# Optimization experiments

Hardware: AMD Instinct MI355X
Metric: run time of the kernel (lower is better)

Reference implementation:

```python
import jax, jax.numpy as jnp
import numpy as np
import math

INF = 100000.0
EPS = 1e-08


def setup_inputs() -> dict:
    key = jax.random.key(0)
    ks = jax.random.split(key, 12)
    B, N, c_n, c_z, C, H, Pq, Pv = 1, 768, 384, 128, 16, 12, 4, 8
    s = jax.random.normal(ks[0], (B, N, c_n), jnp.float32)
    z = jax.random.normal(ks[1], (B, N, N, c_z), jnp.float32)
    # proper rotation-ish frames via QR of random matrices
    m = jax.random.normal(ks[2], (B, N, 3, 3), jnp.float32)
    rot, _ = jnp.linalg.qr(m)
    trans = jax.random.normal(ks[3], (B, N, 3), jnp.float32) * 10.0
    pair_mask = jnp.ones((B, N, N), jnp.float32)

    def lin(k, fin, fout, scale=0.02):
        kw, kb = jax.random.split(k)
        w = jax.random.normal(kw, (fin, fout), jnp.float32) * scale
        b = jax.random.normal(kb, (fout,), jnp.float32) * scale
        return w, b

    wq, bq = lin(ks[4], c_n, H * C)
    wkv, bkv = lin(ks[5], c_n, 2 * H * C)
    wqp, bqp = lin(ks[6], c_n, H * Pq * 3)
    wkvp, bkvp = lin(ks[7], c_n, H * (Pq + Pv) * 3)
    wb, bb = lin(ks[8], c_z, H)
    head_weights = jnp.full((H,), 0.5413248546129181, jnp.float32)  # softplus^-1(1)
    concat_dim = H * (c_z + C + Pv * 4)
    wout, bout = lin(ks[9], concat_dim, c_n)
    return dict(s=s, z=z, rot=rot, trans=trans, pair_mask=pair_mask,
                wq=wq, bq=bq, wkv=wkv, bkv=bkv, wqp=wqp, bqp=bqp,
                wkvp=wkvp, bkvp=bkvp, wb=wb, bb=bb,
                head_weights=head_weights, wout=wout, bout=bout)


def reference(s, z, rot, trans, pair_mask, wq, bq, wkv, bkv, wqp, bqp,
              wkvp, bkvp, wb, bb, head_weights, wout, bout):
    B, N, _ = s.shape
    H = head_weights.shape[0]
    C = wq.shape[1] // H
    Pq = wqp.shape[1] // (3 * H)
    Ptot = wkvp.shape[1] // (3 * H)
    Pv = Ptot - Pq

    q = (s @ wq + bq).reshape(B, N, H, C)
    kv = (s @ wkv + bkv).reshape(B, N, H, 2 * C)
    k, v = kv[..., :C], kv[..., C:]

    def make_pts(x_flat, n):
        # torch: split last dim into 3 contiguous chunks (x..,y..,z..), stack -> [B,N,n,3]
        p = x_flat.reshape(B, N, 3, n).swapaxes(-1, -2)
        return jnp.einsum('bnij,bnpj->bnpi', rot, p) + trans[:, :, None, :]

    q_pts = make_pts(s @ wqp + bqp, H * Pq).reshape(B, N, H, Pq, 3)
    kv_pts = make_pts(s @ wkvp + bkvp, H * Ptot).reshape(B, N, H, Ptot, 3)
    k_pts, v_pts = kv_pts[..., :Pq, :], kv_pts[..., Pq:, :]

    b_bias = z @ wb + bb  # [B,N,N,H]
    a = jnp.einsum('bihc,bjhc->bhij', q, k) * math.sqrt(1.0 / (3 * C))
    a = a + math.sqrt(1.0 / 3.0) * b_bias.transpose(0, 3, 1, 2)

    # point attention: squared distances in global frame  [B,Ni,Nj,H,Pq]
    d2 = jnp.sum((q_pts[:, :, None] - k_pts[:, None]) ** 2, axis=-1)
    hw = jax.nn.softplus(head_weights) * math.sqrt(1.0 / (3.0 * (Pq * 9.0 / 2.0)))
    pt_att = -0.5 * jnp.sum(d2 * hw[:, None], axis=-1)  # [B,Ni,Nj,H]
    a = a + pt_att.transpose(0, 3, 1, 2)
    a = a + (INF * (pair_mask - 1.0))[:, None]
    a = jax.nn.softmax(a, axis=-1)  # [B,H,Ni,Nj]

    o = jnp.einsum('bhij,bjhc->bihc', a, v).reshape(B, N, H * C)

    o_pt = jnp.einsum('bhij,bjhpc->bihpc', a, v_pts)  # [B,N,H,Pv,3]
    # inverse rigid: R^T (x - t)
    o_pt = jnp.einsum('bnij,bnhpi->bnhpj', rot, o_pt - trans[:, :, None, None, :])
    o_pt_norm = jnp.sqrt(jnp.sum(o_pt ** 2, axis=-1) + EPS).reshape(B, N, H * Pv)
    o_pt = o_pt.reshape(B, N, H * Pv, 3)

    o_pair = jnp.einsum('bhij,bijc->bihc', a, z).reshape(B, N, -1)

    cat = jnp.concatenate(
        [o, o_pt[..., 0], o_pt[..., 1], o_pt[..., 2], o_pt_norm, o_pair], axis=-1)
    return cat @ wout + bout
```

## Files before the change

kernel.cpp:

```cpp
#include <hip/hip_runtime.h>
#include <hip/hip_bf16.h>

#define NRES 768
#define NN2  589824
#define CN   384
#define CZ   128
#define CH   16
#define NH   12
#define CATD 2112
#define LSTR 776

template<typename T> __device__ __forceinline__ float cvt(T x);
template<> __device__ __forceinline__ float cvt<float>(float x) { return x; }
template<> __device__ __forceinline__ float cvt<__hip_bfloat16>(__hip_bfloat16 x) { return __bfloat162float(x); }

template<typename T> struct Ld8;
template<> struct Ld8<float> {
    static __device__ __forceinline__ void go(const float* p, float* f) {
        const float4* q = (const float4*)p;
        float4 a = q[0], b = q[1];
        f[0]=a.x; f[1]=a.y; f[2]=a.z; f[3]=a.w;
        f[4]=b.x; f[5]=b.y; f[6]=b.z; f[7]=b.w;
    }
};
template<> struct Ld8<__hip_bfloat16> {
    static __device__ __forceinline__ void go(const __hip_bfloat16* p, float* f) {
        uint4 u = *(const uint4*)p;
        f[0]=__uint_as_float(u.x<<16); f[1]=__uint_as_float(u.x&0xffff0000u);
        f[2]=__uint_as_float(u.y<<16); f[3]=__uint_as_float(u.y&0xffff0000u);
        f[4]=__uint_as_float(u.z<<16); f[5]=__uint_as_float(u.z&0xffff0000u);
        f[6]=__uint_as_float(u.w<<16); f[7]=__uint_as_float(u.w&0xffff0000u);
    }
};

template<typename T> struct Ld4;
template<> struct Ld4<float> {
    static __device__ __forceinline__ void go(const float* p, float* f) {
        float4 a = *(const float4*)p;
        f[0]=a.x; f[1]=a.y; f[2]=a.z; f[3]=a.w;
    }
};
template<> struct Ld4<__hip_bfloat16> {
    static __device__ __forceinline__ void go(const __hip_bfloat16* p, float* f) {
        uint2 u = *(const uint2*)p;
        f[0]=__uint_as_float(u.x<<16); f[1]=__uint_as_float(u.x&0xffff0000u);
        f[2]=__uint_as_float(u.y<<16); f[3]=__uint_as_float(u.y&0xffff0000u);
    }
};

__device__ __forceinline__ bool detect_bf16(const void* pm) {
    const unsigned short* u = (const unsigned short*)pm;
    return (u[0] == 0x3F80u) && (u[1] == 0x3F80u);
}

template<typename T>
__device__ void proj_body(
    const T* __restrict__ s, const T* __restrict__ rot, const T* __restrict__ trans,
    const T* __restrict__ wq, const T* __restrict__ bq,
    const T* __restrict__ wkv, const T* __restrict__ bkv,
    const T* __restrict__ wqp, const T* __restrict__ bqp,
    const T* __restrict__ wkvp, const T* __restrict__ bkvp,
    float* __restrict__ qw, float* __restrict__ kt, float* __restrict__ vw,
    float* __restrict__ qpw, float* __restrict__ kpt, float* __restrict__ vpw,
    float* sL, float* rawL)
{
    const int n0 = blockIdx.x * 4;
    const int tid = threadIdx.x;

    for (int idx = tid; idx < 4 * CN; idx += 256)
        sL[idx] = cvt<T>(s[(size_t)n0 * CN + idx]);
    __syncthreads();

    for (int cq = tid; cq < 288; cq += 256) {
        const int col0 = cq * 4;
        const T* W; int stride, wcol0; const T* Bv;
        if (col0 < 192)      { W = wq;   stride = 192; wcol0 = col0;       Bv = bq;   }
        else if (col0 < 576) { W = wkv;  stride = 384; wcol0 = col0 - 192; Bv = bkv;  }
        else if (col0 < 720) { W = wqp;  stride = 144; wcol0 = col0 - 576; Bv = bqp;  }
        else                 { W = wkvp; stride = 432; wcol0 = col0 - 720; Bv = bkvp; }
        float b4[4];
        Ld4<T>::go(Bv + wcol0, b4);
        float a[4][4];
        #pragma unroll
        for (int r = 0; r < 4; ++r)
            #pragma unroll
            for (int e = 0; e < 4; ++e) a[r][e] = b4[e];
        #pragma unroll 4
        for (int kk = 0; kk < CN; ++kk) {
            float w4[4];
            Ld4<T>::go(W + (size_t)kk * stride + wcol0, w4);
            #pragma unroll
            for (int r = 0; r < 4; ++r) {
                const float sv = sL[r * CN + kk];
                a[r][0] += sv * w4[0];
                a[r][1] += sv * w4[1];
                a[r][2] += sv * w4[2];
                a[r][3] += sv * w4[3];
            }
        }
        #pragma unroll
        for (int e = 0; e < 4; ++e) {
            const int col = col0 + e;
            const int wcol = wcol0 + e;
            #pragma unroll
            for (int r = 0; r < 4; ++r) {
                const int n = n0 + r;
                const float val = a[r][e];
                if (col < 192) {
                    qw[(size_t)n * 192 + col] = val;
                } else if (col < 576) {
                    int hh = wcol >> 5, x = wcol & 31;
                    if (x < 16) kt[(size_t)(hh * 16 + x) * NRES + n] = val;
                    else        vw[(size_t)n * 192 + hh * 16 + (x - 16)] = val;
                } else if (col < 720) {
                    rawL[r * 576 + wcol] = val;
                } else {
                    rawL[r * 576 + 144 + wcol] = val;
                }
            }
        }
    }
    __syncthreads();

    for (int idx = tid; idx < 4 * 192; idx += 256) {
        const int r = idx / 192, p = idx % 192;
        const int n = n0 + r;
        float R[9], Tt[3];
        #pragma unroll
        for (int d = 0; d < 9; ++d) R[d] = cvt<T>(rot[(size_t)n * 9 + d]);
        #pragma unroll
        for (int d = 0; d < 3; ++d) Tt[d] = cvt<T>(trans[(size_t)n * 3 + d]);
        float lx, ly, lz;
        if (p < 48) {
            lx = rawL[r * 576 + p];
            ly = rawL[r * 576 + 48 + p];
            lz = rawL[r * 576 + 96 + p];
        } else {
            const int pk = p - 48;
            lx = rawL[r * 576 + 144 + pk];
            ly = rawL[r * 576 + 144 + 144 + pk];
            lz = rawL[r * 576 + 144 + 288 + pk];
        }
        const float gx = R[0] * lx + R[1] * ly + R[2] * lz + Tt[0];
        const float gy = R[3] * lx + R[4] * ly + R[5] * lz + Tt[1];
        const float gz = R[6] * lx + R[7] * ly + R[8] * lz + Tt[2];
        if (p < 48) {
            float* d = qpw + (size_t)n * 144 + p * 3;
            d[0] = gx; d[1] = gy; d[2] = gz;
        } else {
            const int pk = p - 48;
            const int hh = pk / 12, pp = pk % 12;
            if (pp < 4) {
                const int comp = (hh * 4 + pp) * 3;
                kpt[(size_t)(comp + 0) * NRES + n] = gx;
                kpt[(size_t)(comp + 1) * NRES + n] = gy;
                kpt[(size_t)(comp + 2) * NRES + n] = gz;
            } else {
                float* d = vpw + (size_t)n * 288 + (hh * 8 + (pp - 4)) * 3;
                d[0] = gx; d[1] = gy; d[2] = gz;
            }
        }
    }
}

__global__ __launch_bounds__(256) void k_proj(
    const void* s, const void* rot, const void* trans,
    const void* wq, const void* bq, const void* wkv, const void* bkv,
    const void* wqp, const void* bqp, const void* wkvp, const void* bkvp,
    const void* pm,
    float* qw, float* kt, float* vw, float* qpw, float* kpt, float* vpw)
{
    __shared__ float sL[4 * CN];
    __shared__ float rawL[4 * 576];
    if (detect_bf16(pm))
        proj_body<__hip_bfloat16>((const __hip_bfloat16*)s, (const __hip_bfloat16*)rot,
            (const __hip_bfloat16*)trans, (const __hip_bfloat16*)wq, (const __hip_bfloat16*)bq,
            (const __hip_bfloat16*)wkv, (const __hip_bfloat16*)bkv, (const __hip_bfloat16*)wqp,
            (const __hip_bfloat16*)bqp, (const __hip_bfloat16*)wkvp, (const __hip_bfloat16*)bkvp,
            qw, kt, vw, qpw, kpt, vpw, sL, rawL);
    else
        proj_body<float>((const float*)s, (const float*)rot, (const float*)trans,
            (const float*)wq, (const float*)bq, (const float*)wkv, (const float*)bkv,
            (const float*)wqp, (const float*)bqp, (const float*)wkvp, (const float*)bkvp,
            qw, kt, vw, qpw, kpt, vpw, sL, rawL);
}

template<typename T>
__device__ void bias_body(const T* __restrict__ z, const T* __restrict__ wb,
                          const T* __restrict__ bb, float* __restrict__ biasg,
                          float* zL, float* wbT, float* bbL, float* outL)
{
    const int tid = threadIdx.x;
    const size_t p0 = (size_t)blockIdx.x * 64;

    for (int idx = tid; idx < CZ * NH; idx += 256) {
        const int c = idx / NH, h = idx - c * NH;
        wbT[h * 132 + c] = cvt<T>(wb[idx]);
    }
    if (tid < NH) bbL[tid] = cvt<T>(bb[tid]);

    for (int v8 = tid; v8 < 64 * CZ / 8; v8 += 256) {
        float f[8];
        Ld8<T>::go(z + p0 * CZ + (size_t)v8 * 8, f);
        const int pp = v8 >> 4, cc = (v8 & 15) * 8;
        #pragma unroll
        for (int u = 0; u < 8; ++u) zL[pp * 132 + cc + u] = f[u];
    }
    __syncthreads();

    const float SB = 0.5773502691896258f;
    for (int o = tid; o < 64 * NH; o += 256) {
        const int pp = o / NH, h = o - pp * NH;
        const float* zr = &zL[pp * 132];
        const float* wr = &wbT[h * 132];
        float acc = bbL[h];
        #pragma unroll 8
        for (int c = 0; c < CZ; ++c) acc += zr[c] * wr[c];
        outL[h * 64 + pp] = SB * acc;
    }
    __syncthreads();

    for (int v4 = tid; v4 < 192; v4 += 256) {
        const int h = v4 / 16, pp4 = (v4 - h * 16) * 4;
        *(float4*)(biasg + (size_t)h * NN2 + p0 + pp4) = *(const float4*)&outL[h * 64 + pp4];
    }
}

__global__ __launch_bounds__(256) void k_bias(
    const void* z, const void* wb, const void* bb, const void* pm, float* biasg)
{
    __shared__ float zL[64 * 132];
    __shared__ float wbT[NH * 132];
    __shared__ float bbL[NH];
    __shared__ float outL[NH * 64];
    if (detect_bf16(pm))
        bias_body<__hip_bfloat16>((const __hip_bfloat16*)z, (const __hip_bfloat16*)wb,
                                  (const __hip_bfloat16*)bb, biasg, zL, wbT, bbL, outL);
    else
        bias_body<float>((const float*)z, (const float*)wb, (const float*)bb,
                         biasg, zL, wbT, bbL, outL);
}

template<typename T>
__device__ void attn_split_body(
    const T* __restrict__ pm, const T* __restrict__ hw,
    const float* __restrict__ qw, const float* __restrict__ kt,
    const float* __restrict__ qpw, const float* __restrict__ kpt,
    float* bA,
    float* L, float* qL, float* qpL, float* coefL)
{
    const int i = blockIdx.x, tid = threadIdx.x;

    if (tid < 192) qL[tid] = qw[(size_t)i * 192 + tid];
    if (tid < 144) qpL[tid] = qpw[(size_t)i * 144 + tid];
    if (tid < NH) {
        const float x = cvt<T>(hw[tid]);
        coefL[tid] = -0.5f * log1pf(__expf(x)) * 0.13608276348795434f;
    }
    __syncthreads();

    const float SQK = 0.14433756729740643f;

    for (int t = tid; t < 768; t += 256) {
        const int q = t % 192, g = t / 192;
        const int j0 = 4 * q;
        float mk[4];
        Ld4<T>::go(pm + (size_t)i * NRES + j0, mk);
        #pragma unroll
        for (int e = 0; e < 4; ++e) mk[e] = 100000.0f * (mk[e] - 1.0f);
        #pragma unroll
        for (int hh = 0; hh < 3; ++hh) {
            const int h = 3 * g + hh;
            const float4 b4 = *(const float4*)(bA + (size_t)h * NN2 + (size_t)i * NRES + j0);
            float4 qk = make_float4(0.f, 0.f, 0.f, 0.f);
            #pragma unroll
            for (int c = 0; c < CH; ++c) {
                const float qc = qL[h * CH + c];
                const float4 kv = *(const float4*)(kt + (size_t)(h * CH + c) * NRES + j0);
                qk.x += qc * kv.x; qk.y += qc * kv.y; qk.z += qc * kv.z; qk.w += qc * kv.w;
            }
            float4 dd = make_float4(0.f, 0.f, 0.f, 0.f);
            #pragma unroll
            for (int pc = 0; pc < 12; ++pc) {
                const float qp = qpL[h * 12 + pc];
                const float4 kp = *(const float4*)(kpt + (size_t)(h * 12 + pc) * NRES + j0);
                const float dx = qp - kp.x, dy = qp - kp.y, dz = qp - kp.z, dw = qp - kp.w;
                dd.x += dx * dx; dd.y += dy * dy; dd.z += dz * dz; dd.w += dw * dw;
            }
            const float cf = coefL[h];
            float4 o;
            o.x = SQK * qk.x + b4.x + cf * dd.x + mk[0];
            o.y = SQK * qk.y + b4.y + cf * dd.y + mk[1];
            o.z = SQK * qk.z + b4.z + cf * dd.z + mk[2];
            o.w = SQK * qk.w + b4.w + cf * dd.w + mk[3];
            *(float4*)&L[h * LSTR + j0] = o;
        }
    }
    __syncthreads();

    const int wave = tid >> 6, lane = tid & 63;
    for (int hh = 0; hh < 3; ++hh) {
        const int h = wave * 3 + hh;
        float m = -1e30f;
        for (int j = lane; j < NRES; j += 64) m = fmaxf(m, L[h * LSTR + j]);
        #pragma unroll
        for (int off = 32; off > 0; off >>= 1) m = fmaxf(m, __shfl_xor(m, off));
        float ssum = 0.f;
        for (int j = lane; j < NRES; j += 64) {
            const float e = __expf(L[h * LSTR + j] - m);
            L[h * LSTR + j] = e;
            ssum += e;
        }
        #pragma unroll
        for (int off = 32; off > 0; off >>= 1) ssum += __shfl_xor(ssum, off);
        const float inv = 1.0f / ssum;
        for (int j = lane; j < NRES; j += 64) L[h * LSTR + j] *= inv;
    }
    __syncthreads();

    for (int v = tid; v < 2304; v += 256) {
        const int h = v / 192, q = v - h * 192;
        *(float4*)(bA + (size_t)h * NN2 + (size_t)i * NRES + 4 * q)
            = *(const float4*)&L[h * LSTR + 4 * q];
    }
}

__global__ __launch_bounds__(256, 4) void k_attn_split(
    const void* pm, const void* hw,
    const float* qw, const float* kt, const float* qpw, const float* kpt,
    float* bA)
{
    __shared__ float L[NH * LSTR];
    __shared__ float qL[192];
    __shared__ float qpL[144];
    __shared__ float coefL[NH];
    if (detect_bf16(pm))
        attn_split_body<__hip_bfloat16>((const __hip_bfloat16*)pm,
            (const __hip_bfloat16*)hw, qw, kt, qpw, kpt, bA, L, qL, qpL, coefL);
    else
        attn_split_body<float>((const float*)pm,
            (const float*)hw, qw, kt, qpw, kpt, bA, L, qL, qpL, coefL);
}

template<typename T>
__device__ void av_body(const T* __restrict__ z, const T* __restrict__ rot,
                        const T* __restrict__ trans,
                        const float* __restrict__ Ag,
                        const float* __restrict__ vw, const float* __restrict__ vpw,
                        float* __restrict__ cat, float* buf, float* og)
{
    const int i = blockIdx.x, tid = threadIdx.x;

    for (int v = tid; v < 2304; v += 256) {
        const int h = v / 192, q = v - h * 192;
        const float4 rd = *(const float4*)(Ag + (size_t)h * NN2 + (size_t)i * NRES + 4 * q);
        buf[(4 * q + 0) * NH + h] = rd.x;
        buf[(4 * q + 1) * NH + h] = rd.y;
        buf[(4 * q + 2) * NH + h] = rd.z;
        buf[(4 * q + 3) * NH + h] = rd.w;
    }
    __syncthreads();

    const int lane5 = tid & 31;
    const int jg = tid >> 5;
    const int j0 = jg * 96;

    float4 pacc[NH];
    #pragma unroll
    for (int h = 0; h < NH; ++h) pacc[h] = make_float4(0.f, 0.f, 0.f, 0.f);

    float4 vacc[4];
    const float* vbase[4]; int vstr[4], hsel[4]; bool vok[4];
    #pragma unroll
    for (int k = 0; k < 4; ++k) {
        int m = lane5 + 32 * k;
        vok[k] = (m < 120);
        if (!vok[k]) m = 0;
        const int h = m / 10, q = m - h * 10;
        hsel[k] = h;
        if (q < 4) { vbase[k] = vw  + h * 16 + 4 * q;       vstr[k] = 192; }
        else       { vbase[k] = vpw + h * 24 + 4 * (q - 4); vstr[k] = 288; }
        vacc[k] = make_float4(0.f, 0.f, 0.f, 0.f);
    }

    const T* zr = z + (size_t)i * NRES * CZ;
    for (int j = j0; j < j0 + 96; ++j) {
        float f[4];
        Ld4<T>::go(zr + (size_t)j * CZ + lane5 * 4, f);
        const float4* ar = (const float4*)&buf[j * NH];
        const float4 a0 = ar[0], a1 = ar[1], a2 = ar[2];
        const float av[NH] = {a0.x,a0.y,a0.z,a0.w, a1.x,a1.y,a1.z,a1.w, a2.x,a2.y,a2.z,a2.w};
        #pragma unroll
        for (int h = 0; h < NH; ++h) {
            pacc[h].x += av[h] * f[0];
            pacc[h].y += av[h] * f[1];
            pacc[h].z += av[h] * f[2];
            pacc[h].w += av[h] * f[3];
        }
        #pragma unroll
        for (int k = 0; k < 4; ++k) {
            const float4 vv = *(const float4*)(vbase[k] + (size_t)j * vstr[k]);
            const float a = buf[j * NH + hsel[k]];
            vacc[k].x += a * vv.x;
            vacc[k].y += a * vv.y;
            vacc[k].z += a * vv.z;
            vacc[k].w += a * vv.w;
        }
    }
    __syncthreads();

    #pragma unroll
    for (int h = 0; h < NH; ++h)
        *(float4*)&buf[(jg * NH + h) * CZ + lane5 * 4] = pacc[h];
    __syncthreads();
    float* crow = cat + (size_t)i * CATD + 576;
    for (int o = tid; o < NH * CZ; o += 256) {
        float s = 0.f;
        #pragma unroll
        for (int g = 0; g < 8; ++g) s += buf[g * NH * CZ + o];
        crow[o] = s;
    }
    __syncthreads();

    #pragma unroll
    for (int k = 0; k < 4; ++k)
        if (vok[k]) *(float4*)&buf[jg * 480 + (lane5 + 32 * k) * 4] = vacc[k];
    __syncthreads();
    for (int o = tid; o < 480; o += 256) {
        float s = 0.f;
        #pragma unroll
        for (int g = 0; g < 8; ++g) s += buf[g * 480 + o];
        const int h = o / 40, t = o - h * 40;
        if (t < 16) cat[(size_t)i * CATD + h * 16 + t] = s;
        else        og[h * 24 + (t - 16)] = s;
    }
    __syncthreads();

    if (tid < 96) {
        const int h = tid >> 3, p = tid & 7;
        float R[9], Tt[3];
        #pragma unroll
        for (int d = 0; d < 9; ++d) R[d] = cvt<T>(rot[(size_t)i * 9 + d]);
        #pragma unroll
        for (int d = 0; d < 3; ++d) Tt[d] = cvt<T>(trans[(size_t)i * 3 + d]);
        const float gx = og[h * 24 + p * 3 + 0] - Tt[0];
        const float gy = og[h * 24 + p * 3 + 1] - Tt[1];
        const float gz = og[h * 24 + p * 3 + 2] - Tt[2];
        const float lx = R[0] * gx + R[3] * gy + R[6] * gz;
        const float ly = R[1] * gx + R[4] * gy + R[7] * gz;
        const float lz = R[2] * gx + R[5] * gy + R[8] * gz;
        const float nrm = sqrtf(lx * lx + ly * ly + lz * lz + 1e-8f);
        float* cr = cat + (size_t)i * CATD;
        cr[192 + tid] = lx;
        cr[288 + tid] = ly;
        cr[384 + tid] = lz;
        cr[480 + tid] = nrm;
    }
}

__global__ __launch_bounds__(256) void k_av(
    const void* z, const void* pm, const void* rot, const void* trans,
    const float* Ag, const float* vw, const float* vpw, float* cat)
{
    __shared__ float buf[8 * NH * CZ];
    __shared__ float og[288];
    if (detect_bf16(pm))
        av_body<__hip_bfloat16>((const __hip_bfloat16*)z, (const __hip_bfloat16*)rot,
                                (const __hip_bfloat16*)trans, Ag, vw, vpw, cat, buf, og);
    else
        av_body<float>((const float*)z, (const float*)rot, (const float*)trans,
                       Ag, vw, vpw, cat, buf, og);
}

template<typename T>
__device__ void attn_fused_body(
    const T* __restrict__ z, const T* __restrict__ pm,
    const T* __restrict__ wb, const T* __restrict__ bb, const T* __restrict__ hw,
    const T* __restrict__ rot, const T* __restrict__ trans,
    const float* __restrict__ qw, const float* __restrict__ kt,
    const float* __restrict__ qpw, const float* __restrict__ kpt,
    const float* __restrict__ vw, const float* __restrict__ vpw,
    float* __restrict__ cat,
    float* L, float* wbL, float* qL, float* qpL, float* coefL, float* bbL,
    float* og, float* opairL)
{
    const int i = blockIdx.x, tid = threadIdx.x;

    for (int idx = tid; idx < CZ * NH; idx += 256) wbL[idx] = cvt<T>(wb[idx]);
    if (tid < 192) qL[tid] = qw[(size_t)i * 192 + tid];
    if (tid < 144) qpL[tid] = qpw[(size_t)i * 144 + tid];
    if (tid < NH) {
        const float x = cvt<T>(hw[tid]);
        coefL[tid] = -0.5f * log1pf(__expf(x)) * 0.13608276348795434f;
        bbL[tid] = cvt<T>(bb[tid]);
    }
    __syncthreads();

    const float SQK = 0.14433756729740643f;
    const float SB  = 0.5773502691896258f;

    for (int j = tid; j < NRES; j += 256) {
        const T* zr = z + ((size_t)i * NRES + j) * CZ;
        float bias[NH];
        #pragma unroll
        for (int h = 0; h < NH; ++h) bias[h] = 0.f;
        for (int cb = 0; cb < 16; ++cb) {
            float zf[8];
            Ld8<T>::go(zr + cb * 8, zf);
            #pragma unroll
            for (int uu = 0; uu < 8; ++uu) {
                const float* wrow = &wbL[(cb * 8 + uu) * NH];
                const float zc = zf[uu];
                #pragma unroll
                for (int h = 0; h < NH; ++h) bias[h] += zc * wrow[h];
            }
        }
        const float maskoff = 100000.0f * (cvt<T>(pm[(size_t)i * NRES + j]) - 1.0f);
        #pragma unroll
        for (int h = 0; h < NH; ++h) {
            float qk = 0.f;
            #pragma unroll
            for (int c = 0; c < CH; ++c)
                qk += qL[h * CH + c] * kt[(size_t)(h * CH + c) * NRES + j];
            float d2s = 0.f;
            #pragma unroll
            for (int pc = 0; pc < 12; ++pc) {
                const float diff = qpL[h * 12 + pc] - kpt[(size_t)(h * 12 + pc) * NRES + j];
                d2s += diff * diff;
            }
            L[h * NRES + j] = SQK * qk + SB * (bias[h] + bbL[h]) + coefL[h] * d2s + maskoff;
        }
    }
    __syncthreads();

    const int wave = tid >> 6, lane = tid & 63;
    for (int hh = 0; hh < 3; ++hh) {
        const int h = wave * 3 + hh;
        float m = -1e30f;
        for (int j = lane; j < NRES; j += 64) m = fmaxf(m, L[h * NRES + j]);
        #pragma unroll
        for (int off = 32; off > 0; off >>= 1) m = fmaxf(m, __shfl_xor(m, off));
        float ssum = 0.f;
        for (int j = lane; j < NRES; j += 64) {
            const float e = __expf(L[h * NRES + j] - m);
            L[h * NRES + j] = e;
            ssum += e;
        }
        #pragma unroll
        for (int off = 32; off > 0; off >>= 1) ssum += __shfl_xor(ssum, off);
        const float inv = 1.0f / ssum;
        for (int j = lane; j < NRES; j += 64) L[h * NRES + j] *= inv;
    }
    __syncthreads();

    for (int oc = tid; oc < 480; oc += 256) {
        float acc = 0.f;
        if (oc < 192) {
            const int h = oc >> 4;
            const float* Lh = &L[h * NRES];
            #pragma unroll 4
            for (int j = 0; j < NRES; ++j) acc += Lh[j] * vw[(size_t)j * 192 + oc];
            cat[(size_t)i * CATD + oc] = acc;
        } else {
            const int t = oc - 192;
            const int h = t / 24;
            const float* Lh = &L[h * NRES];
            #pragma unroll 4
            for (int j = 0; j < NRES; ++j) acc += Lh[j] * vpw[(size_t)j * 288 + t];
            og[t] = acc;
        }
    }
    __syncthreads();

    if (tid < 96) {
        const int h = tid >> 3, p = tid & 7;
        float R[9], Tt[3];
        #pragma unroll
        for (int d = 0; d < 9; ++d) R[d] = cvt<T>(rot[(size_t)i * 9 + d]);
        #pragma unroll
        for (int d = 0; d < 3; ++d) Tt[d] = cvt<T>(trans[(size_t)i * 3 + d]);
        const float gx = og[h * 24 + p * 3 + 0] - Tt[0];
        const float gy = og[h * 24 + p * 3 + 1] - Tt[1];
        const float gz = og[h * 24 + p * 3 + 2] - Tt[2];
        const float lx = R[0] * gx + R[3] * gy + R[6] * gz;
        const float ly = R[1] * gx + R[4] * gy + R[7] * gz;
        const float lz = R[2] * gx + R[5] * gy + R[8] * gz;
        const float nrm = sqrtf(lx * lx + ly * ly + lz * lz + 1e-8f);
        float* cr = cat + (size_t)i * CATD;
        cr[192 + tid] = lx;
        cr[288 + tid] = ly;
        cr[384 + tid] = lz;
        cr[480 + tid] = nrm;
    }

    const int c = tid & 127, half = tid >> 7;
    float acc[NH];
    #pragma unroll
    for (int h = 0; h < NH; ++h) acc[h] = 0.f;
    const T* zi = z + (size_t)i * NRES * CZ;
    for (int j = half * 384; j < half * 384 + 384; ++j) {
        const float zv = cvt<T>(zi[(size_t)j * CZ + c]);
        #pragma unroll
        for (int h = 0; h < NH; ++h) acc[h] += L[h * NRES + j] * zv;
    }
    if (half == 0) {
        #pragma unroll
        for (int h = 0; h < NH; ++h) opairL[h * CZ + c] = acc[h];
    }
    __syncthreads();
    if (half == 1) {
        #pragma unroll
        for (int h = 0; h < NH; ++h) opairL[h * CZ + c] += acc[h];
    }
    __syncthreads();
    float* crow = cat + (size_t)i * CATD + 576;
    for (int idx = tid; idx < NH * CZ; idx += 256) crow[idx] = opairL[idx];
}

__global__ __launch_bounds__(256) void k_attn_fused(
    const void* z, const void* pm, const void* wb, const void* bb, const void* hw,
    const void* rot, const void* trans,
    const float* qw, const float* kt, const float* qpw, const float* kpt,
    const float* vw, const float* vpw, float* cat)
{
    __shared__ float L[NH * NRES];
    __shared__ float wbL[CZ * NH];
    __shared__ float qL[192];
    __shared__ float qpL[144];
    __shared__ float coefL[NH], bbL[NH];
    __shared__ float og[288];
    __shared__ float opairL[NH * CZ];
    if (detect_bf16(pm))
        attn_fused_body<__hip_bfloat16>((const __hip_bfloat16*)z, (const __hip_bfloat16*)pm,
            (const __hip_bfloat16*)wb, (const __hip_bfloat16*)bb, (const __hip_bfloat16*)hw,
            (const __hip_bfloat16*)rot, (const __hip_bfloat16*)trans,
            qw, kt, qpw, kpt, vw, vpw, cat, L, wbL, qL, qpL, coefL, bbL, og, opairL);
    else
        attn_fused_body<float>((const float*)z, (const float*)pm,
            (const float*)wb, (const float*)bb, (const float*)hw,
            (const float*)rot, (const float*)trans,
            qw, kt, qpw, kpt, vw, vpw, cat, L, wbL, qL, qpL, coefL, bbL, og, opairL);
}

template<typename T>
__device__ void out_body(const float* __restrict__ cat, const T* __restrict__ wout,
                         const T* __restrict__ bout, T* __restrict__ out,
                         float* catL, float* red)
{
    const int i0 = blockIdx.x * 4, tid = threadIdx.x;
    {
        const float4* src = (const float4*)(cat + (size_t)i0 * CATD);
        float4* dst = (float4*)catL;
        for (int v = tid; v < CATD; v += 384) dst[v] = src[v];
    }
    __syncthreads();

    const int cq = tid % 96, kg = tid / 96;
    const int c0 = cq * 4;
    const int k0 = kg * 528;
    float a[4][4];
    #pragma unroll
    for (int r = 0; r < 4; ++r)
        #pragma unroll
        for (int e = 0; e < 4; ++e) a[r][e] = 0.f;

    #pragma unroll 4
    for (int kk = k0; kk < k0 + 528; ++kk) {
        float w4[4];
        Ld4<T>::go(wout + (size_t)kk * CN + c0, w4);
        #pragma unroll
        for (int r = 0; r < 4; ++r) {
            const float cv = catL[r * CATD + kk];
            a[r][0] += cv * w4[0];
            a[r][1] += cv * w4[1];
            a[r][2] += cv * w4[2];
            a[r][3] += cv * w4[3];
        }
    }
    #pragma unroll
    for (int r = 0; r < 4; ++r)
        *(float4*)&red[(kg * 4 + r) * CN + c0] = make_float4(a[r][0], a[r][1], a[r][2], a[r][3]);
    __syncthreads();

    for (int o = tid; o < 4 * CN; o += 384) {
        const int r = o / CN, col = o - r * CN;
        float s = red[(0 * 4 + r) * CN + col] + red[(1 * 4 + r) * CN + col]
                + red[(2 * 4 + r) * CN + col] + red[(3 * 4 + r) * CN + col];
        out[(size_t)(i0 + r) * CN + col] = (T)(s + cvt<T>(bout[col]));
    }
}

__global__ __launch_bounds__(384) void k_out(
    const float* cat, const void* wout, const void* bout, void* out, const void* pm)
{
    __shared__ float catL[4 * CATD];
    __shared__ float red[16 * CN];
    if (detect_bf16(pm))
        out_body<__hip_bfloat16>(cat, (const __hip_bfloat16*)wout,
                                 (const __hip_bfloat16*)bout, (__hip_bfloat16*)out, catL, red);
    else
        out_body<float>(cat, (const float*)wout, (const float*)bout, (float*)out, catL, red);
}

extern "C" void kernel_launch(void* const* d_in, const int* in_sizes, int n_in,
                              void* d_out, int out_size, void* d_ws, size_t ws_size,
                              hipStream_t stream) {
    const void* s         = d_in[0];
    const void* z         = d_in[1];
    const void* rot       = d_in[2];
    const void* trans     = d_in[3];
    const void* pair_mask = d_in[4];
    const void* wq        = d_in[5];
    const void* bq        = d_in[6];
    const void* wkv       = d_in[7];
    const void* bkv       = d_in[8];
    const void* wqp       = d_in[9];
    const void* bqp       = d_in[10];
    const void* wkvp      = d_in[11];
    const void* bkvp      = d_in[12];
    const void* wb        = d_in[13];
    const void* bb        = d_in[14];
    const void* hw        = d_in[15];
    const void* wout      = d_in[16];
    const void* bout      = d_in[17];

    float* ws  = (float*)d_ws;
    float* qw  = ws;
    float* kt  = qw  + (size_t)NRES * 192;
    float* vw  = kt  + (size_t)NRES * 192;
    float* qpw = vw  + (size_t)NRES * 192;
    float* kpt = qpw + (size_t)NRES * 144;
    float* vpw = kpt + (size_t)NRES * 144;
    float* cat = vpw + (size_t)NRES * 288;
    float* bA  = cat + (size_t)NRES * CATD;

    const size_t need_split = ((size_t)2506752 + 7077888) * sizeof(float);

    k_proj<<<NRES / 4, 256, 0, stream>>>(s, rot, trans, wq, bq, wkv, bkv,
                                         wqp, bqp, wkvp, bkvp, pair_mask,
                                         qw, kt, vw, qpw, kpt, vpw);
    if (ws_size >= need_split) {
        k_bias<<<(NRES * NRES) / 64, 256, 0, stream>>>(z, wb, bb, pair_mask, bA);
        k_attn_split<<<NRES, 256, 0, stream>>>(pair_mask, hw,
                                               qw, kt, qpw, kpt, bA);
        k_av<<<NRES, 256, 0, stream>>>(z, pair_mask, rot, trans,
                                       bA, vw, vpw, cat);
    } else {
        k_attn_fused<<<NRES, 256, 0, stream>>>(z, pair_mask, wb, bb, hw, rot, trans,
                                               qw, kt, qpw, kpt, vw, vpw, cat);
    }
    k_out<<<NRES / 4, 384, 0, stream>>>(cat, wout, bout, d_out, pair_mask);
}
```

Before: 850.1 us.

## Retile projection, bias and output kernels for more parallelism and register reuse

The projection kernel now gives each block a single residue instead of four, launching 768 blocks for more parallelism at the cost of reloading the weights four times as often. The pair-bias kernel drops its shared-memory staging of z: each thread keeps a quarter of a row in registers and the partial dot products are combined with warp shuffles. The output GEMM moves to 8 columns per thread with float4 reads from shared memory, splits K eight ways and reduces in two stages. Several shared arrays gain 16-byte alignment so the vector accesses are valid.

```diff
diff --git a/kernel.cpp b/kernel.cpp
--- a/kernel.cpp
+++ b/kernel.cpp
@@ -64,11 +64,11 @@
     float* __restrict__ qpw, float* __restrict__ kpt, float* __restrict__ vpw,
     float* sL, float* rawL)
 {
-    const int n0 = blockIdx.x * 4;
+    const int n = blockIdx.x;
     const int tid = threadIdx.x;
 
-    for (int idx = tid; idx < 4 * CN; idx += 256)
-        sL[idx] = cvt<T>(s[(size_t)n0 * CN + idx]);
+    for (int idx = tid; idx < CN; idx += 256)
+        sL[idx] = cvt<T>(s[(size_t)n * CN + idx]);
     __syncthreads();
 
     for (int cq = tid; cq < 288; cq += 256) {
@@ -78,53 +78,39 @@
         else if (col0 < 576) { W = wkv;  stride = 384; wcol0 = col0 - 192; Bv = bkv;  }
         else if (col0 < 720) { W = wqp;  stride = 144; wcol0 = col0 - 576; Bv = bqp;  }
         else                 { W = wkvp; stride = 432; wcol0 = col0 - 720; Bv = bkvp; }
-        float b4[4];
-        Ld4<T>::go(Bv + wcol0, b4);
-        float a[4][4];
-        #pragma unroll
-        for (int r = 0; r < 4; ++r)
-            #pragma unroll
-            for (int e = 0; e < 4; ++e) a[r][e] = b4[e];
-        #pragma unroll 4
+        float a[4];
+        Ld4<T>::go(Bv + wcol0, a);
+        #pragma unroll 8
         for (int kk = 0; kk < CN; ++kk) {
             float w4[4];
             Ld4<T>::go(W + (size_t)kk * stride + wcol0, w4);
-            #pragma unroll
-            for (int r = 0; r < 4; ++r) {
-                const float sv = sL[r * CN + kk];
-                a[r][0] += sv * w4[0];
-                a[r][1] += sv * w4[1];
-                a[r][2] += sv * w4[2];
-                a[r][3] += sv * w4[3];
-            }
+            const float sv = sL[kk];
+            a[0] += sv * w4[0];
+            a[1] += sv * w4[1];
+            a[2] += sv * w4[2];
+            a[3] += sv * w4[3];
         }
         #pragma unroll
         for (int e = 0; e < 4; ++e) {
             const int col = col0 + e;
             const int wcol = wcol0 + e;
-            #pragma unroll
-            for (int r = 0; r < 4; ++r) {
-                const int n = n0 + r;
-                const float val = a[r][e];
-                if (col < 192) {
-                    qw[(size_t)n * 192 + col] = val;
-                } else if (col < 576) {
-                    int hh = wcol >> 5, x = wcol & 31;
-                    if (x < 16) kt[(size_t)(hh * 16 + x) * NRES + n] = val;
-                    else        vw[(size_t)n * 192 + hh * 16 + (x - 16)] = val;
-                } else if (col < 720) {
-                    rawL[r * 576 + wcol] = val;
-                } else {
-                    rawL[r * 576 + 144 + wcol] = val;
-                }
+            const float val = a[e];
+            if (col < 192) {
+                qw[(size_t)n * 192 + col] = val;
+            } else if (col < 576) {
+                int hh = wcol >> 5, x = wcol & 31;
+                if (x < 16) kt[(size_t)(hh * 16 + x) * NRES + n] = val;
+                else        vw[(size_t)n * 192 + hh * 16 + (x - 16)] = val;
+            } else if (col < 720) {
+                rawL[wcol] = val;
+            } else {
+                rawL[144 + wcol] = val;
             }
         }
     }
     __syncthreads();
 
-    for (int idx = tid; idx < 4 * 192; idx += 256) {
-        const int r = idx / 192, p = idx % 192;
-        const int n = n0 + r;
+    for (int p = tid; p < 192; p += 256) {
         float R[9], Tt[3];
         #pragma unroll
         for (int d = 0; d < 9; ++d) R[d] = cvt<T>(rot[(size_t)n * 9 + d]);
@@ -132,14 +118,14 @@
         for (int d = 0; d < 3; ++d) Tt[d] = cvt<T>(trans[(size_t)n * 3 + d]);
         float lx, ly, lz;
         if (p < 48) {
-            lx = rawL[r * 576 + p];
-            ly = rawL[r * 576 + 48 + p];
-            lz = rawL[r * 576 + 96 + p];
+            lx = rawL[p];
+            ly = rawL[48 + p];
+            lz = rawL[96 + p];
         } else {
             const int pk = p - 48;
-            lx = rawL[r * 576 + 144 + pk];
-            ly = rawL[r * 576 + 144 + 144 + pk];
-            lz = rawL[r * 576 + 144 + 288 + pk];
+            lx = rawL[144 + pk];
+            ly = rawL[144 + 144 + pk];
+            lz = rawL[144 + 288 + pk];
         }
         const float gx = R[0] * lx + R[1] * ly + R[2] * lz + Tt[0];
         const float gy = R[3] * lx + R[4] * ly + R[5] * lz + Tt[1];
@@ -170,8 +156,8 @@
     const void* pm,
     float* qw, float* kt, float* vw, float* qpw, float* kpt, float* vpw)
 {
-    __shared__ float sL[4 * CN];
-    __shared__ float rawL[4 * 576];
+    __shared__ __attribute__((aligned(16))) float sL[CN];
+    __shared__ __attribute__((aligned(16))) float rawL[576];
     if (detect_bf16(pm))
         proj_body<__hip_bfloat16>((const __hip_bfloat16*)s, (const __hip_bfloat16*)rot,
             (const __hip_bfloat16*)trans, (const __hip_bfloat16*)wq, (const __hip_bfloat16*)bq,
@@ -188,7 +174,7 @@
 template<typename T>
 __device__ void bias_body(const T* __restrict__ z, const T* __restrict__ wb,
                           const T* __restrict__ bb, float* __restrict__ biasg,
-                          float* zL, float* wbT, float* bbL, float* outL)
+                          float* wbT, float* bbL, float* outL)
 {
     const int tid = threadIdx.x;
     const size_t p0 = (size_t)blockIdx.x * 64;
@@ -199,24 +185,36 @@
     }
     if (tid < NH) bbL[tid] = cvt<T>(bb[tid]);
 
-    for (int v8 = tid; v8 < 64 * CZ / 8; v8 += 256) {
-        float f[8];
-        Ld8<T>::go(z + p0 * CZ + (size_t)v8 * 8, f);
-        const int pp = v8 >> 4, cc = (v8 & 15) * 8;
-        #pragma unroll
-        for (int u = 0; u < 8; ++u) zL[pp * 132 + cc + u] = f[u];
-    }
-    __syncthreads();
-
+    const int pp = tid >> 2, qq = tid & 3;
+    float zreg[32];
+    #pragma unroll
+    for (int u = 0; u < 4; ++u)
+        Ld8<T>::go(z + (p0 + pp) * CZ + qq * 32 + u * 8, zreg + u * 8);
+    __syncthreads();
+
+    const float4* wbT4 = (const float4*)wbT;
+    float acc[NH];
+    #pragma unroll
+    for (int h = 0; h < NH; ++h) acc[h] = 0.f;
+    #pragma unroll
+    for (int h = 0; h < NH; ++h) {
+        #pragma unroll
+        for (int c4 = 0; c4 < 8; ++c4) {
+            const float4 w = wbT4[h * 33 + qq * 8 + c4];
+            acc[h] += zreg[c4 * 4 + 0] * w.x + zreg[c4 * 4 + 1] * w.y
+                    + zreg[c4 * 4 + 2] * w.z + zreg[c4 * 4 + 3] * w.w;
+        }
+    }
+    #pragma unroll
+    for (int h = 0; h < NH; ++h) {
+        acc[h] += __shfl_xor(acc[h], 1);
+        acc[h] += __shfl_xor(acc[h], 2);
+    }
     const float SB = 0.5773502691896258f;
-    for (int o = tid; o < 64 * NH; o += 256) {
-        const int pp = o / NH, h = o - pp * NH;
-        const float* zr = &zL[pp * 132];
-        const float* wr = &wbT[h * 132];
-        float acc = bbL[h];
-        #pragma unroll 8
-        for (int c = 0; c < CZ; ++c) acc += zr[c] * wr[c];
-        outL[h * 64 + pp] = SB * acc;
+    if (qq == 0) {
+        #pragma unroll
+        for (int h = 0; h < NH; ++h)
+            outL[h * 64 + pp] = SB * (acc[h] + bbL[h]);
     }
     __syncthreads();
 
@@ -229,16 +227,15 @@
 __global__ __launch_bounds__(256) void k_bias(
     const void* z, const void* wb, const void* bb, const void* pm, float* biasg)
 {
-    __shared__ float zL[64 * 132];
-    __shared__ float wbT[NH * 132];
+    __shared__ __attribute__((aligned(16))) float wbT[NH * 132];
     __shared__ float bbL[NH];
-    __shared__ float outL[NH * 64];
+    __shared__ __attribute__((aligned(16))) float outL[NH * 64];
     if (detect_bf16(pm))
         bias_body<__hip_bfloat16>((const __hip_bfloat16*)z, (const __hip_bfloat16*)wb,
-                                  (const __hip_bfloat16*)bb, biasg, zL, wbT, bbL, outL);
+                                  (const __hip_bfloat16*)bb, biasg, wbT, bbL, outL);
     else
         bias_body<float>((const float*)z, (const float*)wb, (const float*)bb,
-                         biasg, zL, wbT, bbL, outL);
+                         biasg, wbT, bbL, outL);
 }
 
 template<typename T>
@@ -330,7 +327,7 @@
     const float* qw, const float* kt, const float* qpw, const float* kpt,
     float* bA)
 {
-    __shared__ float L[NH * LSTR];
+    __shared__ __attribute__((aligned(16))) float L[NH * LSTR];
     __shared__ float qL[192];
     __shared__ float qpL[144];
     __shared__ float coefL[NH];
@@ -462,7 +459,7 @@
     const void* z, const void* pm, const void* rot, const void* trans,
     const float* Ag, const float* vw, const float* vpw, float* cat)
 {
-    __shared__ float buf[8 * NH * CZ];
+    __shared__ __attribute__((aligned(16))) float buf[8 * NH * CZ];
     __shared__ float og[288];
     if (detect_bf16(pm))
         av_body<__hip_bfloat16>((const __hip_bfloat16*)z, (const __hip_bfloat16*)rot,
@@ -655,31 +652,54 @@
     }
     __syncthreads();
 
-    const int cq = tid % 96, kg = tid / 96;
-    const int c0 = cq * 4;
-    const int k0 = kg * 528;
-    float a[4][4];
+    const int oct = tid % 48, kg = tid / 48;
+    const int c0 = oct * 8;
+    const int k0 = kg * 264;
+
+    float a[4][8];
     #pragma unroll
     for (int r = 0; r < 4; ++r)
         #pragma unroll
-        for (int e = 0; e < 4; ++e) a[r][e] = 0.f;
-
-    #pragma unroll 4
-    for (int kk = k0; kk < k0 + 528; ++kk) {
-        float w4[4];
-        Ld4<T>::go(wout + (size_t)kk * CN + c0, w4);
+        for (int e = 0; e < 8; ++e) a[r][e] = 0.f;
+
+    for (int kb = 0; kb < 264; kb += 4) {
+        float4 cv[4];
+        #pragma unroll
+        for (int r = 0; r < 4; ++r)
+            cv[r] = *(const float4*)&catL[r * CATD + k0 + kb];
+        #pragma unroll
+        for (int u = 0; u < 4; ++u) {
+            float w8[8];
+            Ld8<T>::go(wout + (size_t)(k0 + kb + u) * CN + c0, w8);
+            #pragma unroll
+            for (int r = 0; r < 4; ++r) {
+                const float cvru = (u == 0) ? cv[r].x : (u == 1) ? cv[r].y
+                                 : (u == 2) ? cv[r].z : cv[r].w;
+                #pragma unroll
+                for (int e = 0; e < 8; ++e) a[r][e] += cvru * w8[e];
+            }
+        }
+    }
+
+    if (kg < 4) {
         #pragma unroll
         for (int r = 0; r < 4; ++r) {
-            const float cv = catL[r * CATD + kk];
-            a[r][0] += cv * w4[0];
-            a[r][1] += cv * w4[1];
-            a[r][2] += cv * w4[2];
-            a[r][3] += cv * w4[3];
-        }
-    }
-    #pragma unroll
-    for (int r = 0; r < 4; ++r)
-        *(float4*)&red[(kg * 4 + r) * CN + c0] = make_float4(a[r][0], a[r][1], a[r][2], a[r][3]);
+            *(float4*)&red[(kg * 4 + r) * CN + c0]     = make_float4(a[r][0], a[r][1], a[r][2], a[r][3]);
+            *(float4*)&red[(kg * 4 + r) * CN + c0 + 4] = make_float4(a[r][4], a[r][5], a[r][6], a[r][7]);
+        }
+    }
+    __syncthreads();
+    if (kg >= 4) {
+        #pragma unroll
+        for (int r = 0; r < 4; ++r) {
+            float4* p0 = (float4*)&red[((kg - 4) * 4 + r) * CN + c0];
+            float4* p1 = (float4*)&red[((kg - 4) * 4 + r) * CN + c0 + 4];
+            float4 v0 = *p0, v1 = *p1;
+            v0.x += a[r][0]; v0.y += a[r][1]; v0.z += a[r][2]; v0.w += a[r][3];
+            v1.x += a[r][4]; v1.y += a[r][5]; v1.z += a[r][6]; v1.w += a[r][7];
+            *p0 = v0; *p1 = v1;
+        }
+    }
     __syncthreads();
 
     for (int o = tid; o < 4 * CN; o += 384) {
@@ -693,8 +713,8 @@
 __global__ __launch_bounds__(384) void k_out(
     const float* cat, const void* wout, const void* bout, void* out, const void* pm)
 {
-    __shared__ float catL[4 * CATD];
-    __shared__ float red[16 * CN];
+    __shared__ __attribute__((aligned(16))) float catL[4 * CATD];
+    __shared__ __attribute__((aligned(16))) float red[16 * CN];
     if (detect_bf16(pm))
         out_body<__hip_bfloat16>(cat, (const __hip_bfloat16*)wout,
                                  (const __hip_bfloat16*)bout, (__hip_bfloat16*)out, catL, red);
@@ -736,9 +756,9 @@
 
     const size_t need_split = ((size_t)2506752 + 7077888) * sizeof(float);
 
-    k_proj<<<NRES / 4, 256, 0, stream>>>(s, rot, trans, wq, bq, wkv, bkv,
-                                         wqp, bqp, wkvp, bkvp, pair_mask,
-                                         qw, kt, vw, qpw, kpt, vpw);
+    k_proj<<<NRES, 256, 0, stream>>>(s, rot, trans, wq, bq, wkv, bkv,
+                                     wqp, bqp, wkvp, bkvp, pair_mask,
+                                     qw, kt, vw, qpw, kpt, vpw);
     if (ws_size >= need_split) {
         k_bias<<<(NRES * NRES) / 64, 256, 0, stream>>>(z, wb, bb, pair_mask, bA);
         k_attn_split<<<NRES, 256, 0, stream>>>(pair_mask, hw,
```

New measurement: 709.0 us. 1.2x faster.
